# Performance work log

Hardware: AMD Instinct MI355X
Metric: run time of the kernel (lower is better)

Reference implementation:

```python
import jax, jax.numpy as jnp
import numpy as np

B, N, E, H = 1, 4096, 256, 4
D = E // H  # 64


def setup_inputs() -> dict:
    key = jax.random.key(0)
    ks = jax.random.split(key, 16)
    s = lambda fan_in: 1.0 / np.sqrt(fan_in)
    inp = {
        "x": jax.random.normal(ks[0], (B, N, E), dtype=jnp.float32),
        "encoding": jax.random.normal(ks[1], (2, 1, 1, N, D), dtype=jnp.float32),
        # Wqkv: Linear(E, 3E)
        "Wqkv_w": jax.random.uniform(ks[2], (3 * E, E), jnp.float32, -s(E), s(E)),
        "Wqkv_b": jax.random.uniform(ks[3], (3 * E,), jnp.float32, -s(E), s(E)),
        # out_proj: Linear(E, E)
        "out_w": jax.random.uniform(ks[4], (E, E), jnp.float32, -s(E), s(E)),
        "out_b": jax.random.uniform(ks[5], (E,), jnp.float32, -s(E), s(E)),
        # ffn[0]: Linear(2E, 2E)
        "ffn1_w": jax.random.uniform(ks[6], (2 * E, 2 * E), jnp.float32, -s(2 * E), s(2 * E)),
        "ffn1_b": jax.random.uniform(ks[7], (2 * E,), jnp.float32, -s(2 * E), s(2 * E)),
        # ffn[1]: LayerNorm(2E)
        "ln_g": jnp.ones((2 * E,), jnp.float32),
        "ln_b": jnp.zeros((2 * E,), jnp.float32),
        # ffn[3]: Linear(2E, E)
        "ffn2_w": jax.random.uniform(ks[8], (E, 2 * E), jnp.float32, -s(2 * E), s(2 * E)),
        "ffn2_b": jax.random.uniform(ks[9], (E,), jnp.float32, -s(2 * E), s(2 * E)),
    }
    return inp


def _rotate_half(t):
    # t: (B, H, N, D) -> pairwise rotate along last dim
    t2 = t.reshape(B, H, -1, D // 2, 2)
    t2 = jnp.stack((-t2[..., 1], t2[..., 0]), axis=-1)
    return t2.reshape(B, H, -1, D)


def _layernorm(x, g, b, eps=1e-5):
    mu = jnp.mean(x, axis=-1, keepdims=True)
    var = jnp.mean(jnp.square(x - mu), axis=-1, keepdims=True)
    return (x - mu) * jax.lax.rsqrt(var + eps) * g + b


def reference(x, encoding, Wqkv_w, Wqkv_b, out_w, out_b,
              ffn1_w, ffn1_b, ln_g, ln_b, ffn2_w, ffn2_b):
    # fused QKV projection; last dim layout is (H, D, 3)
    qkv = x @ Wqkv_w.T + Wqkv_b                       # (B, N, 3E)
    qkv = qkv.reshape(B, N, H, D, 3).transpose(0, 2, 1, 3, 4)  # (B, H, N, D, 3)
    q, k, v = qkv[..., 0], qkv[..., 1], qkv[..., 2]
    # cached rotary embedding: t*cos + rotate_half(t)*sin
    q = q * encoding[0] + _rotate_half(q) * encoding[1]
    k = k * encoding[0] + _rotate_half(k) * encoding[1]
    # scaled dot-product attention (no mask)
    scores = jnp.einsum("bhqd,bhkd->bhqk", q, k) / np.sqrt(D).astype(np.float32)
    probs = jax.nn.softmax(scores, axis=-1)
    ctx = jnp.einsum("bhqk,bhkd->bhqd", probs, v)     # (B, H, N, D)
    ctx = ctx.transpose(0, 2, 1, 3).reshape(B, N, E)
    message = ctx @ out_w.T + out_b
    # concat-FFN with residual
    h = jnp.concatenate((x, message), axis=-1)        # (B, N, 2E)
    h = h @ ffn1_w.T + ffn1_b
    h = _layernorm(h, ln_g, ln_b)
    h = jax.nn.gelu(h, approximate=False)
    h = h @ ffn2_w.T + ffn2_b
    return x + h
```

## Files before the change

kernel.cpp:

```cpp
#include <hip/hip_runtime.h>
#include <math.h>

#define NTOK 4096
#define EMB  256
#define NH   4
#define HD   64

typedef unsigned short u16;
typedef __attribute__((ext_vector_type(8))) __bf16 bf16x8;
typedef __attribute__((ext_vector_type(4))) float f32x4;

__device__ __forceinline__ u16 f2bf(float f) {
    union { float f; unsigned u; } v; v.f = f;
    unsigned b = v.u;
    b += 0x7FFFu + ((b >> 16) & 1u);
    return (u16)(b >> 16);
}
__device__ __forceinline__ float bf2f(u16 u) {
    union { unsigned u; float f; } v; v.u = ((unsigned)u) << 16;
    return v.f;
}

__global__ __launch_bounds__(256) void prep(
    const float4* __restrict__ w0, const float4* __restrict__ w1,
    const float4* __restrict__ w2, const float4* __restrict__ w3,
    u16* __restrict__ wb,
    const float4* __restrict__ x4, u16* __restrict__ xb, u16* __restrict__ catb)
{
    const int bid = blockIdx.x;
    if (bid < 640) {
        const int f = bid * 256 + threadIdx.x;
        float4 v;
        if      (f <  49152) v = w0[f];
        else if (f <  65536) v = w1[f - 49152];
        else if (f < 131072) v = w2[f - 65536];
        else                 v = w3[f - 131072];
        uint2 o;
        o.x = (unsigned)f2bf(v.x) | ((unsigned)f2bf(v.y) << 16);
        o.y = (unsigned)f2bf(v.z) | ((unsigned)f2bf(v.w) << 16);
        *(uint2*)(wb + (size_t)f * 4) = o;
    } else {
        const int f = (bid - 640) * 256 + threadIdx.x;
        float4 v = x4[f];
        uint2 o;
        o.x = (unsigned)f2bf(v.x) | ((unsigned)f2bf(v.y) << 16);
        o.y = (unsigned)f2bf(v.z) | ((unsigned)f2bf(v.w) << 16);
        *(uint2*)(xb + (size_t)f * 4) = o;
        const int row = f >> 6, c = (f & 63) * 4;
        *(uint2*)(catb + (size_t)row * 512 + c) = o;
    }
}

__global__ __launch_bounds__(256) void gemm_bf16_abt(
    const u16* __restrict__ A,
    const u16* __restrict__ B,
    const float* __restrict__ bias,
    const float* __restrict__ resid, int ldr,
    float* __restrict__ Cf, u16* __restrict__ Cb, int ldc, int K)
{
    const int t = threadIdx.x, w = t >> 6, l = t & 63;
    const int lg = l >> 4, li = l & 15;
    const int row0 = blockIdx.y * 64 + w * 16;
    const int col0 = blockIdx.x * 64;

    f32x4 acc[4];
    #pragma unroll
    for (int nb = 0; nb < 4; ++nb) acc[nb] = (f32x4){0.f, 0.f, 0.f, 0.f};

    const u16* Ap = A + (size_t)(row0 + li) * K + lg * 8;
    const u16* Bp = B + (size_t)(col0 + li) * K + lg * 8;

    #pragma unroll 2
    for (int k0 = 0; k0 < K; k0 += 32) {
        bf16x8 a = *(const bf16x8*)(Ap + k0);
        #pragma unroll
        for (int nb = 0; nb < 4; ++nb) {
            bf16x8 b = *(const bf16x8*)(Bp + (size_t)nb * 16 * K + k0);
            acc[nb] = __builtin_amdgcn_mfma_f32_16x16x32_bf16(a, b, acc[nb], 0, 0, 0);
        }
    }

    #pragma unroll
    for (int nb = 0; nb < 4; ++nb) {
        const int col = col0 + nb * 16 + li;
        const float bs = bias[col];
        #pragma unroll
        for (int p = 0; p < 4; ++p) {
            const int row = row0 + lg * 4 + p;
            float v = acc[nb][p] + bs;
            if (resid) v += resid[(size_t)row * ldr + col];
            if (Cf) Cf[(size_t)row * ldc + col] = v;
            else    Cb[(size_t)row * ldc + col] = f2bf(v);
        }
    }
}

__global__ __launch_bounds__(256) void qkv_post(
    const u16* __restrict__ qkvb, const float* __restrict__ enc,
    unsigned* __restrict__ Qb, unsigned* __restrict__ Kb, u16* __restrict__ Vt)
{
    const int bid = blockIdx.x;
    if (bid < 2048) {
        const int gid = bid * 256 + threadIdx.x;
        const int h   = gid >> 17;
        const int rem = gid & (NTOK * 32 - 1);
        const int n   = rem >> 5;
        const int p   = rem & 31;
        const int d0  = p * 2;

        const u16* base = qkvb + (size_t)n * 768 + h * 192 + d0 * 3;
        const float q0v = bf2f(base[0]), k0 = bf2f(base[1]);
        const float q1  = bf2f(base[3]), k1 = bf2f(base[4]);

        float2 c01 = *(const float2*)(enc + (size_t)n * 64 + d0);
        float2 s01 = *(const float2*)(enc + (size_t)NTOK * 64 + (size_t)n * 64 + d0);

        const float qo0 = (q0v * c01.x - q1 * s01.x) * 0.125f;
        const float qo1 = (q1 * c01.y + q0v * s01.y) * 0.125f;
        const float ko0 = k0 * c01.x - k1 * s01.x;
        const float ko1 = k1 * c01.y + k0 * s01.y;

        const size_t oidx = ((size_t)(h * NTOK + n) << 5) + p;
        Qb[oidx] = (unsigned)f2bf(qo0) | ((unsigned)f2bf(qo1) << 16);
        Kb[oidx] = (unsigned)f2bf(ko0) | ((unsigned)f2bf(ko1) << 16);
    } else {
        const int vb = bid - 2048;
        const int h  = vb >> 6;
        const int nt = vb & 63;
        const int t  = threadIdx.x;
        const int d  = t & 63;
        const int nc = t >> 6;

        __align__(16) u16 us[16];
        #pragma unroll
        for (int i = 0; i < 16; ++i) {
            const int n = nt * 64 + nc * 16 + i;
            us[i] = qkvb[(size_t)n * 768 + h * 192 + d * 3 + 2];
        }
        u16* dst = Vt + ((size_t)(h * 64 + d) << 12) + nt * 64 + nc * 16;
        *(uint4*)(dst)     = *(uint4*)(us);
        *(uint4*)(dst + 8) = *(uint4*)(us + 8);
    }
}

__global__ __launch_bounds__(512, 2) void flash_attn_v3(
    const u16* __restrict__ Qb, const u16* __restrict__ Kb,
    const u16* __restrict__ Vt, u16* __restrict__ ctxb)
{
    __shared__ char  Plds[8 * 4096];
    __shared__ float Obuf[32 * 64];
    __shared__ float Mbuf[32], Lbuf[32];

    const int t  = threadIdx.x;
    const int wk = t >> 6;
    const int l  = t & 63;
    const int lg = l >> 4, li = l & 15;
    const int h  = blockIdx.y;
    const int q0 = blockIdx.x * 32;

    char* Pw = Plds + wk * 4096;

    bf16x8 QA[2][2];
    #pragma unroll
    for (int Mb = 0; Mb < 2; ++Mb)
        #pragma unroll
        for (int kh = 0; kh < 2; ++kh)
            QA[Mb][kh] = *(const bf16x8*)(Qb +
                ((size_t)(h * NTOK + q0 + Mb * 16 + li) << 6) + kh * 32 + lg * 8);

    f32x4 OA[2][4];
    float mrun[2][4], lrun[2][4];
    #pragma unroll
    for (int Mb = 0; Mb < 2; ++Mb) {
        #pragma unroll
        for (int p = 0; p < 4; ++p) { mrun[Mb][p] = -1e30f; lrun[Mb][p] = 0.f; }
        #pragma unroll
        for (int db = 0; db < 4; ++db) OA[Mb][db] = (f32x4){0.f, 0.f, 0.f, 0.f};
    }

    for (int it = 0; it < 8; ++it) {
        const int kt = (wk << 9) + (it << 6);

        bf16x8 KB[4][2], VB[4][2];
        #pragma unroll
        for (int kb = 0; kb < 4; ++kb)
            #pragma unroll
            for (int kh = 0; kh < 2; ++kh)
                KB[kb][kh] = *(const bf16x8*)(Kb +
                    ((size_t)(h * NTOK + kt + kb * 16 + li) << 6) + kh * 32 + lg * 8);
        #pragma unroll
        for (int db = 0; db < 4; ++db)
            #pragma unroll
            for (int kh = 0; kh < 2; ++kh)
                VB[db][kh] = *(const bf16x8*)(Vt +
                    ((size_t)(h * 64 + db * 16 + li) << 12) + kt + kh * 32 + lg * 8);

        f32x4 SA[2][4];
        #pragma unroll
        for (int Mb = 0; Mb < 2; ++Mb)
            #pragma unroll
            for (int kb = 0; kb < 4; ++kb) {
                f32x4 z = (f32x4){0.f, 0.f, 0.f, 0.f};
                z = __builtin_amdgcn_mfma_f32_16x16x32_bf16(QA[Mb][0], KB[kb][0], z, 0, 0, 0);
                SA[Mb][kb] = __builtin_amdgcn_mfma_f32_16x16x32_bf16(QA[Mb][1], KB[kb][1], z, 0, 0, 0);
            }

        #pragma unroll
        for (int Mb = 0; Mb < 2; ++Mb)
            #pragma unroll
            for (int p = 0; p < 4; ++p) {
                float mx = fmaxf(fmaxf(SA[Mb][0][p], SA[Mb][1][p]),
                                 fmaxf(SA[Mb][2][p], SA[Mb][3][p]));
                #pragma unroll
                for (int sh = 1; sh < 16; sh <<= 1)
                    mx = fmaxf(mx, __shfl_xor(mx, sh));
                const float mo = mrun[Mb][p];
                const float mn = fmaxf(mo, mx);
                const float corr = __expf(mo - mn);
                mrun[Mb][p] = mn;
                float pv[4], ps = 0.f;
                #pragma unroll
                for (int kb = 0; kb < 4; ++kb) {
                    pv[kb] = __expf(SA[Mb][kb][p] - mn);
                    ps += pv[kb];
                }
                lrun[Mb][p] = lrun[Mb][p] * corr + ps;
                #pragma unroll
                for (int db = 0; db < 4; ++db) OA[Mb][db][p] *= corr;

                const int ql = Mb * 16 + lg * 4 + p;
                #pragma unroll
                for (int kb = 0; kb < 4; ++kb) {
                    const int kl = kb * 16 + li;
                    *(u16*)(Pw + ql * 128 + ((kl * 2) ^ ((ql & 7) << 4))) = f2bf(pv[kb]);
                }
            }

        #pragma unroll
        for (int Mb = 0; Mb < 2; ++Mb)
            #pragma unroll
            for (int kh = 0; kh < 2; ++kh) {
                const int ql = Mb * 16 + li;
                bf16x8 PA = *(const bf16x8*)(Pw + ql * 128 +
                                ((kh * 64 + lg * 16) ^ ((ql & 7) << 4)));
                #pragma unroll
                for (int db = 0; db < 4; ++db)
                    OA[Mb][db] = __builtin_amdgcn_mfma_f32_16x16x32_bf16(
                        PA, VB[db][kh], OA[Mb][db], 0, 0, 0);
            }
    }

    #pragma unroll
    for (int Mb = 0; Mb < 2; ++Mb)
        #pragma unroll
        for (int p = 0; p < 4; ++p) {
            float ps = lrun[Mb][p];
            #pragma unroll
            for (int sh = 1; sh < 16; sh <<= 1) ps += __shfl_xor(ps, sh);
            lrun[Mb][p] = ps;
        }

    if (wk == 0) {
        #pragma unroll
        for (int Mb = 0; Mb < 2; ++Mb)
            #pragma unroll
            for (int p = 0; p < 4; ++p) {
                const int q = Mb * 16 + lg * 4 + p;
                #pragma unroll
                for (int db = 0; db < 4; ++db)
                    Obuf[q * 64 + db * 16 + li] = OA[Mb][db][p];
                if (li == 0) { Mbuf[q] = mrun[Mb][p]; Lbuf[q] = lrun[Mb][p]; }
            }
    }
    #pragma unroll
    for (int wv = 1; wv < 8; ++wv) {
        __syncthreads();
        if (wk == wv) {
            #pragma unroll
            for (int Mb = 0; Mb < 2; ++Mb)
                #pragma unroll
                for (int p = 0; p < 4; ++p) {
                    const int q = Mb * 16 + lg * 4 + p;
                    const float Mo = Mbuf[q], Lo = Lbuf[q];
                    const float mn = fmaxf(Mo, mrun[Mb][p]);
                    const float a  = __expf(Mo - mn);
                    const float b  = __expf(mrun[Mb][p] - mn);
                    #pragma unroll
                    for (int db = 0; db < 4; ++db) {
                        const int idx = q * 64 + db * 16 + li;
                        Obuf[idx] = Obuf[idx] * a + OA[Mb][db][p] * b;
                    }
                    if (li == 0) { Mbuf[q] = mn; Lbuf[q] = Lo * a + lrun[Mb][p] * b; }
                }
        }
    }
    __syncthreads();

    {
        const int q = t >> 4, dc = (t & 15) * 4;
        const float rl = 1.f / Lbuf[q];
        uint2 ov;
        ov.x = (unsigned)f2bf(Obuf[q * 64 + dc + 0] * rl) |
               ((unsigned)f2bf(Obuf[q * 64 + dc + 1] * rl) << 16);
        ov.y = (unsigned)f2bf(Obuf[q * 64 + dc + 2] * rl) |
               ((unsigned)f2bf(Obuf[q * 64 + dc + 3] * rl) << 16);
        *(uint2*)(ctxb + (size_t)(q0 + q) * EMB + h * 64 + dc) = ov;
    }
}

__global__ __launch_bounds__(256) void ln_gelu(
    const float* __restrict__ h1, const float* __restrict__ g,
    const float* __restrict__ b, u16* __restrict__ h2b)
{
    __shared__ float red[8];
    const int row = blockIdx.x, t = threadIdx.x;
    const float v0 = h1[(size_t)row * 512 + t];
    const float v1 = h1[(size_t)row * 512 + 256 + t];

    float s = v0 + v1;
    #pragma unroll
    for (int w = 1; w < 64; w <<= 1) s += __shfl_xor(s, w);
    if ((t & 63) == 0) red[t >> 6] = s;
    __syncthreads();
    const float mu = (red[0] + red[1] + red[2] + red[3]) * (1.f / 512.f);

    const float d0 = v0 - mu, d1 = v1 - mu;
    float vs = d0 * d0 + d1 * d1;
    #pragma unroll
    for (int w = 1; w < 64; w <<= 1) vs += __shfl_xor(vs, w);
    if ((t & 63) == 0) red[4 + (t >> 6)] = vs;
    __syncthreads();
    const float var  = (red[4] + red[5] + red[6] + red[7]) * (1.f / 512.f);
    const float rstd = rsqrtf(var + 1e-5f);

    const float y0 = d0 * rstd * g[t] + b[t];
    const float y1 = d1 * rstd * g[t + 256] + b[t + 256];
    const float o0 = 0.5f * y0 * (1.f + erff(y0 * 0.70710678118654752f));
    const float o1 = 0.5f * y1 * (1.f + erff(y1 * 0.70710678118654752f));
    h2b[(size_t)row * 512 + t]       = f2bf(o0);
    h2b[(size_t)row * 512 + 256 + t] = f2bf(o1);
}

extern "C" void kernel_launch(void* const* d_in, const int* in_sizes, int n_in,
                              void* d_out, int out_size, void* d_ws, size_t ws_size,
                              hipStream_t stream)
{
    const float* x      = (const float*)d_in[0];
    const float* enc    = (const float*)d_in[1];
    const float* Wqkv_w = (const float*)d_in[2];
    const float* Wqkv_b = (const float*)d_in[3];
    const float* out_w  = (const float*)d_in[4];
    const float* out_b  = (const float*)d_in[5];
    const float* ffn1_w = (const float*)d_in[6];
    const float* ffn1_b = (const float*)d_in[7];
    const float* ln_g   = (const float*)d_in[8];
    const float* ln_b   = (const float*)d_in[9];
    const float* ffn2_w = (const float*)d_in[10];
    const float* ffn2_b = (const float*)d_in[11];
    float* out = (float*)d_out;
    float* ws  = (float*)d_ws;

    u16*   catb = (u16*)(ws);
    u16*   wb   = (u16*)(ws + 1048576);
    u16*   Qb   = (u16*)(ws + 1376256);
    u16*   Kb   = (u16*)(ws + 1900544);
    u16*   Vt   = (u16*)(ws + 2424832);
    u16*   ctxb = (u16*)(ws + 2949120);
    u16*   qkvb = (u16*)(ws + 3473408);
    float* h1   = ws + 3473408;
    u16*   xb   = (u16*)(ws + 5570560);
    u16*   h2b  = (u16*)(ws + 5570560);

    u16* Wqkvb = wb;
    u16* outwb = wb + 196608;
    u16* ffn1b = wb + 262144;
    u16* ffn2b = wb + 524288;

    prep<<<1664, 256, 0, stream>>>((const float4*)Wqkv_w, (const float4*)out_w,
                                   (const float4*)ffn1_w, (const float4*)ffn2_w, wb,
                                   (const float4*)x, xb, catb);
    gemm_bf16_abt<<<dim3(12, 64), 256, 0, stream>>>(xb, Wqkvb, Wqkv_b,
                                                    nullptr, 0, nullptr, qkvb, 768, 256);
    qkv_post<<<2304, 256, 0, stream>>>(qkvb, enc, (unsigned*)Qb, (unsigned*)Kb, Vt);
    flash_attn_v3<<<dim3(128, NH), 512, 0, stream>>>(Qb, Kb, Vt, ctxb);
    gemm_bf16_abt<<<dim3(4, 64), 256, 0, stream>>>(ctxb, outwb, out_b,
                                                   nullptr, 0, nullptr, catb + 256, 512, 256);
    gemm_bf16_abt<<<dim3(8, 64), 256, 0, stream>>>(catb, ffn1b, ffn1_b,
                                                   nullptr, 0, h1, nullptr, 512, 512);
    ln_gelu<<<4096, 256, 0, stream>>>(h1, ln_g, ln_b, h2b);
    gemm_bf16_abt<<<dim3(4, 64), 256, 0, stream>>>(h2b, ffn2b, ffn2_b,
                                                   x, 256, out, nullptr, 256, 512);
}
```

Measured before the change: 239.5 us.

## Retile flash attention to 16-query blocks, LDS-transpose V, bf16 LayerNorm input

Flash attention now runs 16 queries per block with 4 waves, each wave covering 1024 keys, and launches twice as many blocks to raise occupancy. The V transpose in qkv_post is staged through shared memory so both the global reads and the global writes are coalesced. The FFN1 GEMM now writes bf16 instead of fp32, and LayerNorm+GELU handles one row per wave with vector loads and no block barriers. Storing the FFN1 output in bf16 halves that traffic but adds rounding before the normalization. The smaller query tile means K and V are loaded from global memory more times in total.

```diff
diff --git a/kernel.cpp b/kernel.cpp
--- a/kernel.cpp
+++ b/kernel.cpp
@@ -99,6 +99,7 @@
     const u16* __restrict__ qkvb, const float* __restrict__ enc,
     unsigned* __restrict__ Qb, unsigned* __restrict__ Kb, u16* __restrict__ Vt)
 {
+    __shared__ u16 lds[64 * 66];
     const int bid = blockIdx.x;
     if (bid < 2048) {
         const int gid = bid * 256 + threadIdx.x;
@@ -128,58 +129,59 @@
         const int h  = vb >> 6;
         const int nt = vb & 63;
         const int t  = threadIdx.x;
-        const int d  = t & 63;
-        const int nc = t >> 6;
-
-        __align__(16) u16 us[16];
-        #pragma unroll
-        for (int i = 0; i < 16; ++i) {
-            const int n = nt * 64 + nc * 16 + i;
-            us[i] = qkvb[(size_t)n * 768 + h * 192 + d * 3 + 2];
-        }
-        u16* dst = Vt + ((size_t)(h * 64 + d) << 12) + nt * 64 + nc * 16;
-        *(uint4*)(dst)     = *(uint4*)(us);
-        *(uint4*)(dst + 8) = *(uint4*)(us + 8);
-    }
-}
-
-__global__ __launch_bounds__(512, 2) void flash_attn_v3(
+
+        {
+            const int nl = t & 63, dg = t >> 6;
+            const u16* src = qkvb + (size_t)(nt * 64 + nl) * 768 + h * 192 + dg * 48 + 2;
+            #pragma unroll
+            for (int i = 0; i < 16; ++i)
+                lds[(dg * 16 + i) * 66 + nl] = src[3 * i];
+        }
+        __syncthreads();
+        {
+            const int d = t >> 2, nc = t & 3;
+            __align__(16) u16 us[16];
+            #pragma unroll
+            for (int i = 0; i < 16; ++i) us[i] = lds[d * 66 + nc * 16 + i];
+            u16* dst = Vt + ((size_t)(h * 64 + d) << 12) + nt * 64 + nc * 16;
+            *(uint4*)(dst)     = *(uint4*)(us);
+            *(uint4*)(dst + 8) = *(uint4*)(us + 8);
+        }
+    }
+}
+
+__global__ __launch_bounds__(256, 4) void flash_attn_v4(
     const u16* __restrict__ Qb, const u16* __restrict__ Kb,
     const u16* __restrict__ Vt, u16* __restrict__ ctxb)
 {
-    __shared__ char  Plds[8 * 4096];
-    __shared__ float Obuf[32 * 64];
-    __shared__ float Mbuf[32], Lbuf[32];
+    __shared__ char  Plds[4 * 2048];
+    __shared__ float Obuf[16 * 64];
+    __shared__ float Mbuf[16], Lbuf[16];
 
     const int t  = threadIdx.x;
     const int wk = t >> 6;
     const int l  = t & 63;
     const int lg = l >> 4, li = l & 15;
     const int h  = blockIdx.y;
-    const int q0 = blockIdx.x * 32;
-
-    char* Pw = Plds + wk * 4096;
-
-    bf16x8 QA[2][2];
-    #pragma unroll
-    for (int Mb = 0; Mb < 2; ++Mb)
-        #pragma unroll
-        for (int kh = 0; kh < 2; ++kh)
-            QA[Mb][kh] = *(const bf16x8*)(Qb +
-                ((size_t)(h * NTOK + q0 + Mb * 16 + li) << 6) + kh * 32 + lg * 8);
-
-    f32x4 OA[2][4];
-    float mrun[2][4], lrun[2][4];
-    #pragma unroll
-    for (int Mb = 0; Mb < 2; ++Mb) {
-        #pragma unroll
-        for (int p = 0; p < 4; ++p) { mrun[Mb][p] = -1e30f; lrun[Mb][p] = 0.f; }
-        #pragma unroll
-        for (int db = 0; db < 4; ++db) OA[Mb][db] = (f32x4){0.f, 0.f, 0.f, 0.f};
-    }
-
-    for (int it = 0; it < 8; ++it) {
-        const int kt = (wk << 9) + (it << 6);
+    const int q0 = blockIdx.x * 16;
+
+    char* Pw = Plds + wk * 2048;
+
+    bf16x8 QA[2];
+    #pragma unroll
+    for (int kh = 0; kh < 2; ++kh)
+        QA[kh] = *(const bf16x8*)(Qb +
+            ((size_t)(h * NTOK + q0 + li) << 6) + kh * 32 + lg * 8);
+
+    f32x4 OA[4];
+    float mrun[4], lrun[4];
+    #pragma unroll
+    for (int p = 0; p < 4; ++p) { mrun[p] = -1e30f; lrun[p] = 0.f; }
+    #pragma unroll
+    for (int db = 0; db < 4; ++db) OA[db] = (f32x4){0.f, 0.f, 0.f, 0.f};
+
+    for (int it = 0; it < 16; ++it) {
+        const int kt = (wk << 10) + (it << 6);
 
         bf16x8 KB[4][2], VB[4][2];
         #pragma unroll
@@ -195,103 +197,90 @@
                 VB[db][kh] = *(const bf16x8*)(Vt +
                     ((size_t)(h * 64 + db * 16 + li) << 12) + kt + kh * 32 + lg * 8);
 
-        f32x4 SA[2][4];
-        #pragma unroll
-        for (int Mb = 0; Mb < 2; ++Mb)
+        f32x4 SA[4];
+        #pragma unroll
+        for (int kb = 0; kb < 4; ++kb) {
+            f32x4 z = (f32x4){0.f, 0.f, 0.f, 0.f};
+            z = __builtin_amdgcn_mfma_f32_16x16x32_bf16(QA[0], KB[kb][0], z, 0, 0, 0);
+            SA[kb] = __builtin_amdgcn_mfma_f32_16x16x32_bf16(QA[1], KB[kb][1], z, 0, 0, 0);
+        }
+
+        #pragma unroll
+        for (int p = 0; p < 4; ++p) {
+            float mx = fmaxf(fmaxf(SA[0][p], SA[1][p]), fmaxf(SA[2][p], SA[3][p]));
+            #pragma unroll
+            for (int sh = 1; sh < 16; sh <<= 1)
+                mx = fmaxf(mx, __shfl_xor(mx, sh));
+            const float mo = mrun[p];
+            const float mn = fmaxf(mo, mx);
+            const float corr = __expf(mo - mn);
+            mrun[p] = mn;
+            float pv[4], ps = 0.f;
             #pragma unroll
             for (int kb = 0; kb < 4; ++kb) {
-                f32x4 z = (f32x4){0.f, 0.f, 0.f, 0.f};
-                z = __builtin_amdgcn_mfma_f32_16x16x32_bf16(QA[Mb][0], KB[kb][0], z, 0, 0, 0);
-                SA[Mb][kb] = __builtin_amdgcn_mfma_f32_16x16x32_bf16(QA[Mb][1], KB[kb][1], z, 0, 0, 0);
+                pv[kb] = __expf(SA[kb][p] - mn);
+                ps += pv[kb];
             }
-
-        #pragma unroll
-        for (int Mb = 0; Mb < 2; ++Mb)
-            #pragma unroll
-            for (int p = 0; p < 4; ++p) {
-                float mx = fmaxf(fmaxf(SA[Mb][0][p], SA[Mb][1][p]),
-                                 fmaxf(SA[Mb][2][p], SA[Mb][3][p]));
-                #pragma unroll
-                for (int sh = 1; sh < 16; sh <<= 1)
-                    mx = fmaxf(mx, __shfl_xor(mx, sh));
-                const float mo = mrun[Mb][p];
-                const float mn = fmaxf(mo, mx);
-                const float corr = __expf(mo - mn);
-                mrun[Mb][p] = mn;
-                float pv[4], ps = 0.f;
-                #pragma unroll
-                for (int kb = 0; kb < 4; ++kb) {
-                    pv[kb] = __expf(SA[Mb][kb][p] - mn);
-                    ps += pv[kb];
-                }
-                lrun[Mb][p] = lrun[Mb][p] * corr + ps;
-                #pragma unroll
-                for (int db = 0; db < 4; ++db) OA[Mb][db][p] *= corr;
-
-                const int ql = Mb * 16 + lg * 4 + p;
-                #pragma unroll
-                for (int kb = 0; kb < 4; ++kb) {
-                    const int kl = kb * 16 + li;
-                    *(u16*)(Pw + ql * 128 + ((kl * 2) ^ ((ql & 7) << 4))) = f2bf(pv[kb]);
-                }
+            lrun[p] = lrun[p] * corr + ps;
+            #pragma unroll
+            for (int db = 0; db < 4; ++db) OA[db][p] *= corr;
+
+            const int ql = lg * 4 + p;
+            #pragma unroll
+            for (int kb = 0; kb < 4; ++kb) {
+                const int kl = kb * 16 + li;
+                *(u16*)(Pw + ql * 128 + ((kl * 2) ^ ((ql & 7) << 4))) = f2bf(pv[kb]);
             }
-
-        #pragma unroll
-        for (int Mb = 0; Mb < 2; ++Mb)
-            #pragma unroll
-            for (int kh = 0; kh < 2; ++kh) {
-                const int ql = Mb * 16 + li;
-                bf16x8 PA = *(const bf16x8*)(Pw + ql * 128 +
-                                ((kh * 64 + lg * 16) ^ ((ql & 7) << 4)));
-                #pragma unroll
-                for (int db = 0; db < 4; ++db)
-                    OA[Mb][db] = __builtin_amdgcn_mfma_f32_16x16x32_bf16(
-                        PA, VB[db][kh], OA[Mb][db], 0, 0, 0);
-            }
-    }
-
-    #pragma unroll
-    for (int Mb = 0; Mb < 2; ++Mb)
+        }
+
+        #pragma unroll
+        for (int kh = 0; kh < 2; ++kh) {
+            const int ql = li;
+            bf16x8 PA = *(const bf16x8*)(Pw + ql * 128 +
+                            ((kh * 64 + lg * 16) ^ ((ql & 7) << 4)));
+            #pragma unroll
+            for (int db = 0; db < 4; ++db)
+                OA[db] = __builtin_amdgcn_mfma_f32_16x16x32_bf16(
+                    PA, VB[db][kh], OA[db], 0, 0, 0);
+        }
+    }
+
+    #pragma unroll
+    for (int p = 0; p < 4; ++p) {
+        float ps = lrun[p];
+        #pragma unroll
+        for (int sh = 1; sh < 16; sh <<= 1) ps += __shfl_xor(ps, sh);
+        lrun[p] = ps;
+    }
+
+    if (wk == 0) {
         #pragma unroll
         for (int p = 0; p < 4; ++p) {
-            float ps = lrun[Mb][p];
-            #pragma unroll
-            for (int sh = 1; sh < 16; sh <<= 1) ps += __shfl_xor(ps, sh);
-            lrun[Mb][p] = ps;
-        }
-
-    if (wk == 0) {
-        #pragma unroll
-        for (int Mb = 0; Mb < 2; ++Mb)
-            #pragma unroll
-            for (int p = 0; p < 4; ++p) {
-                const int q = Mb * 16 + lg * 4 + p;
-                #pragma unroll
-                for (int db = 0; db < 4; ++db)
-                    Obuf[q * 64 + db * 16 + li] = OA[Mb][db][p];
-                if (li == 0) { Mbuf[q] = mrun[Mb][p]; Lbuf[q] = lrun[Mb][p]; }
-            }
-    }
-    #pragma unroll
-    for (int wv = 1; wv < 8; ++wv) {
+            const int q = lg * 4 + p;
+            #pragma unroll
+            for (int db = 0; db < 4; ++db)
+                Obuf[q * 64 + db * 16 + li] = OA[db][p];
+            if (li == 0) { Mbuf[q] = mrun[p]; Lbuf[q] = lrun[p]; }
+        }
+    }
+    #pragma unroll
+    for (int wv = 1; wv < 4; ++wv) {
         __syncthreads();
         if (wk == wv) {
             #pragma unroll
-            for (int Mb = 0; Mb < 2; ++Mb)
+            for (int p = 0; p < 4; ++p) {
+                const int q = lg * 4 + p;
+                const float Mo = Mbuf[q], Lo = Lbuf[q];
+                const float mn = fmaxf(Mo, mrun[p]);
+                const float a  = __expf(Mo - mn);
+                const float b  = __expf(mrun[p] - mn);
                 #pragma unroll
-                for (int p = 0; p < 4; ++p) {
-                    const int q = Mb * 16 + lg * 4 + p;
-                    const float Mo = Mbuf[q], Lo = Lbuf[q];
-                    const float mn = fmaxf(Mo, mrun[Mb][p]);
-                    const float a  = __expf(Mo - mn);
-                    const float b  = __expf(mrun[Mb][p] - mn);
-                    #pragma unroll
-                    for (int db = 0; db < 4; ++db) {
-                        const int idx = q * 64 + db * 16 + li;
-                        Obuf[idx] = Obuf[idx] * a + OA[Mb][db][p] * b;
-                    }
-                    if (li == 0) { Mbuf[q] = mn; Lbuf[q] = Lo * a + lrun[Mb][p] * b; }
+                for (int db = 0; db < 4; ++db) {
+                    const int idx = q * 64 + db * 16 + li;
+                    Obuf[idx] = Obuf[idx] * a + OA[db][p] * b;
                 }
+                if (li == 0) { Mbuf[q] = mn; Lbuf[q] = Lo * a + lrun[p] * b; }
+            }
         }
     }
     __syncthreads();
@@ -308,37 +297,54 @@
     }
 }
 
-__global__ __launch_bounds__(256) void ln_gelu(
-    const float* __restrict__ h1, const float* __restrict__ g,
+__global__ __launch_bounds__(256) void ln_gelu_v2(
+    const u16* __restrict__ h1b, const float* __restrict__ g,
     const float* __restrict__ b, u16* __restrict__ h2b)
 {
-    __shared__ float red[8];
-    const int row = blockIdx.x, t = threadIdx.x;
-    const float v0 = h1[(size_t)row * 512 + t];
-    const float v1 = h1[(size_t)row * 512 + 256 + t];
-
-    float s = v0 + v1;
-    #pragma unroll
-    for (int w = 1; w < 64; w <<= 1) s += __shfl_xor(s, w);
-    if ((t & 63) == 0) red[t >> 6] = s;
-    __syncthreads();
-    const float mu = (red[0] + red[1] + red[2] + red[3]) * (1.f / 512.f);
-
-    const float d0 = v0 - mu, d1 = v1 - mu;
-    float vs = d0 * d0 + d1 * d1;
-    #pragma unroll
-    for (int w = 1; w < 64; w <<= 1) vs += __shfl_xor(vs, w);
-    if ((t & 63) == 0) red[4 + (t >> 6)] = vs;
-    __syncthreads();
-    const float var  = (red[4] + red[5] + red[6] + red[7]) * (1.f / 512.f);
-    const float rstd = rsqrtf(var + 1e-5f);
-
-    const float y0 = d0 * rstd * g[t] + b[t];
-    const float y1 = d1 * rstd * g[t + 256] + b[t + 256];
-    const float o0 = 0.5f * y0 * (1.f + erff(y0 * 0.70710678118654752f));
-    const float o1 = 0.5f * y1 * (1.f + erff(y1 * 0.70710678118654752f));
-    h2b[(size_t)row * 512 + t]       = f2bf(o0);
-    h2b[(size_t)row * 512 + 256 + t] = f2bf(o1);
+    const int wid = threadIdx.x >> 6, l = threadIdx.x & 63;
+    const int row = blockIdx.x * 4 + wid;
+
+    uint4 hv = *(const uint4*)(h1b + (size_t)row * 512 + l * 8);
+    const unsigned* hw = (const unsigned*)&hv;
+    float v[8];
+    #pragma unroll
+    for (int j = 0; j < 4; ++j) {
+        v[2 * j]     = bf2f((u16)(hw[j] & 0xffff));
+        v[2 * j + 1] = bf2f((u16)(hw[j] >> 16));
+    }
+
+    float s = 0.f;
+    #pragma unroll
+    for (int i = 0; i < 8; ++i) s += v[i];
+    #pragma unroll
+    for (int sh = 1; sh < 64; sh <<= 1) s += __shfl_xor(s, sh);
+    const float mu = s * (1.f / 512.f);
+
+    float d[8], vs = 0.f;
+    #pragma unroll
+    for (int i = 0; i < 8; ++i) { d[i] = v[i] - mu; vs += d[i] * d[i]; }
+    #pragma unroll
+    for (int sh = 1; sh < 64; sh <<= 1) vs += __shfl_xor(vs, sh);
+    const float rstd = rsqrtf(vs * (1.f / 512.f) + 1e-5f);
+
+    float4 g0 = *(const float4*)(g + l * 8);
+    float4 g1 = *(const float4*)(g + l * 8 + 4);
+    float4 b0 = *(const float4*)(b + l * 8);
+    float4 b1 = *(const float4*)(b + l * 8 + 4);
+    float gg[8] = {g0.x, g0.y, g0.z, g0.w, g1.x, g1.y, g1.z, g1.w};
+    float bb[8] = {b0.x, b0.y, b0.z, b0.w, b1.x, b1.y, b1.z, b1.w};
+
+    uint4 ov;
+    unsigned* op = (unsigned*)&ov;
+    #pragma unroll
+    for (int j = 0; j < 4; ++j) {
+        float y0 = d[2 * j] * rstd * gg[2 * j] + bb[2 * j];
+        float y1 = d[2 * j + 1] * rstd * gg[2 * j + 1] + bb[2 * j + 1];
+        float o0 = 0.5f * y0 * (1.f + erff(y0 * 0.70710678118654752f));
+        float o1 = 0.5f * y1 * (1.f + erff(y1 * 0.70710678118654752f));
+        op[j] = (unsigned)f2bf(o0) | ((unsigned)f2bf(o1) << 16);
+    }
+    *(uint4*)(h2b + (size_t)row * 512 + l * 8) = ov;
 }
 
 extern "C" void kernel_launch(void* const* d_in, const int* in_sizes, int n_in,
@@ -367,7 +373,7 @@
     u16*   Vt   = (u16*)(ws + 2424832);
     u16*   ctxb = (u16*)(ws + 2949120);
     u16*   qkvb = (u16*)(ws + 3473408);
-    float* h1   = ws + 3473408;
+    u16*   h1b  = (u16*)(ws + 3473408);
     u16*   xb   = (u16*)(ws + 5570560);
     u16*   h2b  = (u16*)(ws + 5570560);
 
@@ -382,12 +388,12 @@
     gemm_bf16_abt<<<dim3(12, 64), 256, 0, stream>>>(xb, Wqkvb, Wqkv_b,
                                                     nullptr, 0, nullptr, qkvb, 768, 256);
     qkv_post<<<2304, 256, 0, stream>>>(qkvb, enc, (unsigned*)Qb, (unsigned*)Kb, Vt);
-    flash_attn_v3<<<dim3(128, NH), 512, 0, stream>>>(Qb, Kb, Vt, ctxb);
+    flash_attn_v4<<<dim3(256, NH), 256, 0, stream>>>(Qb, Kb, Vt, ctxb);
     gemm_bf16_abt<<<dim3(4, 64), 256, 0, stream>>>(ctxb, outwb, out_b,
                                                    nullptr, 0, nullptr, catb + 256, 512, 256);
     gemm_bf16_abt<<<dim3(8, 64), 256, 0, stream>>>(catb, ffn1b, ffn1_b,
-                                                   nullptr, 0, h1, nullptr, 512, 512);
-    ln_gelu<<<4096, 256, 0, stream>>>(h1, ln_g, ln_b, h2b);
+                                                   nullptr, 0, nullptr, h1b, 512, 512);
+    ln_gelu_v2<<<1024, 256, 0, stream>>>(h1b, ln_g, ln_b, h2b);
     gemm_bf16_abt<<<dim3(4, 64), 256, 0, stream>>>(h2b, ffn2b, ffn2_b,
                                                    x, 256, out, nullptr, 256, 512);
 }
```

After: 280.8 us. +17.2%, slower.
